# Performance work log

Hardware: AMD Instinct MI355X
Metric: run time of the kernel (lower is better)

Reference implementation:

```python
import jax, jax.numpy as jnp
import numpy as np

B, S, D, K, DF, H, DFF = 2, 512, 512, 8, 64, 8, 2048
DH = D // H  # d_head = 64
CS = D // K  # chunk_size = 64


def layer_norm(x, g, b, eps=1e-5):
    m = x.mean(-1, keepdims=True)
    v = ((x - m) ** 2).mean(-1, keepdims=True)
    return (x - m) / jnp.sqrt(v + eps) * g + b


def matexp_taylor(M, terms=6):
    # exp(M) ~= I + M + M^2/2! + ... (6 terms), batched over leading dims
    I = jnp.broadcast_to(jnp.eye(M.shape[-1], dtype=M.dtype), M.shape)
    res, P = I, I
    for n in range(1, terms + 1):
        P = jnp.matmul(P, M) / n
        res = res + P
    return res


def setup_inputs() -> dict:
    key = jax.random.key(0)
    ks = jax.random.split(key, 24)
    w = lambda k, shape, s=0.02: (jax.random.normal(k, shape, jnp.float32) * s)
    return {
        'x': jax.random.normal(ks[0], (B, S, D), jnp.float32),
        'u': jax.random.normal(ks[1], (B, S, DF), jnp.float32),
        'Wq': w(ks[2], (D, D)), 'bq': jnp.zeros((D,), jnp.float32),
        'Wk': w(ks[3], (D, D)), 'bk': jnp.zeros((D,), jnp.float32),
        'Wv': w(ks[4], (D, D)), 'bv': jnp.zeros((D,), jnp.float32),
        'Wo': w(ks[5], (D, D)), 'bo': jnp.zeros((D,), jnp.float32),
        'Wfp': w(ks[6], (DF, D)), 'bfp': jnp.zeros((D,), jnp.float32),
        'Wfo': w(ks[7], (D, DF)), 'bfo': jnp.zeros((DF,), jnp.float32),
        'Wc1': w(ks[8], (D, DFF)), 'bc1': jnp.zeros((DFF,), jnp.float32),
        'g_ln': jnp.ones((DFF,), jnp.float32), 'b_ln': jnp.zeros((DFF,), jnp.float32),
        # small scale keeps the Lie elements O(1) so the Taylor matexp is well-behaved
        'Wc2': w(ks[9], (DFF, D * K * K), 0.001), 'bc2': jnp.zeros((D * K * K,), jnp.float32),
    }


def reference(x, u, Wq, bq, Wk, bk, Wv, bv, Wo, bo, Wfp, bfp, Wfo, bfo,
              Wc1, bc1, g_ln, b_ln, Wc2, bc2):
    b, s, d = x.shape
    # --- ConnectionNetwork: A[b,s,d,k,k] ---
    h = jax.nn.gelu(x @ Wc1 + bc1, approximate=False)
    h = layer_norm(h, g_ln, b_ln)
    A = (h @ Wc2 + bc2).reshape(b, s, d, K, K)
    # --- ParallelTransport: lie[b,i,j] = sum_d (x_i - x_j)_d * A[j,d]  ---
    # (split into x_i.A_j and x_j.A_j terms to avoid [b,s,s,d,k,k] intermediate)
    lie = jnp.einsum('bid,bjdkl->bijkl', x, A) - jnp.einsum('bjd,bjdkl->bjkl', x, A)[:, None]
    Gamma = matexp_taylor(-lie)  # [b,s,s,k,k], Gamma[b,i,j] transports j->i
    # --- standard multi-head attention on x (eval mode, no dropout, no mask) ---
    q = (x @ Wq + bq).reshape(b, s, H, DH).transpose(0, 2, 1, 3)
    k_ = (x @ Wk + bk).reshape(b, s, H, DH).transpose(0, 2, 1, 3)
    v = (x @ Wv + bv).reshape(b, s, H, DH).transpose(0, 2, 1, 3)
    scores = jnp.einsum('bhid,bhjd->bhij', q, k_) / jnp.sqrt(jnp.float32(DH))
    attn = jax.nn.softmax(scores, axis=-1)
    ctx = jnp.einsum('bhij,bhjd->bhid', attn, v).transpose(0, 2, 1, 3).reshape(b, s, d)
    x_out = x + ctx @ Wo + bo
    # --- fiber transport: u_i += sum_j attn_avg[i,j] * Gamma[i,j] @ u_chunks[j] ---
    u_proj = u @ Wfp + bfp                      # [b,s,D]
    u_chunks = u_proj.reshape(b, s, K, CS)      # [b,s,k,cs]
    attn_avg = attn.mean(axis=1)                # [b,s,s]
    weighted = Gamma * attn_avg[..., None, None]
    u_t = jnp.einsum('bijkl,bjlc->bikc', weighted, u_chunks).reshape(b, s, d)
    u_out = u + u_t @ Wfo + bfo
    return (x_out, u_out)
```

## Files before the change

kernel.cpp:

```cpp
#include <hip/hip_runtime.h>
#include <math.h>

#define BB 2
#define SS 512
#define DD 512
#define HH 8
#define DFF 2048

typedef __attribute__((ext_vector_type(8))) short bf16x8;
typedef __attribute__((ext_vector_type(4))) float f32x4;

__device__ __forceinline__ float gelu_exact(float v) {
    return 0.5f * v * (1.0f + erff(v * 0.70710678118654752f));
}
__device__ __forceinline__ unsigned short f2bf(float f) {
    unsigned u = __float_as_uint(f);
    u += 0x7FFF + ((u >> 16) & 1);
    return (unsigned short)(u >> 16);
}
__device__ __forceinline__ float bf2f(unsigned short s) {
    return __uint_as_float(((unsigned)s) << 16);
}
__device__ __forceinline__ void gload16(const void* g, void* l) {
    __builtin_amdgcn_global_load_lds((const __attribute__((address_space(1))) void*)g,
                                     (__attribute__((address_space(3))) void*)l, 16, 0, 0);
}

template<int NT, int EPI, int SK = 1>
__global__ __launch_bounds__(256)
void mgemm_k(const unsigned short* __restrict__ A, const unsigned short* __restrict__ B,
             const float* __restrict__ bias, const float* __restrict__ resid,
             float* __restrict__ Cf, unsigned short* __restrict__ Cb,
             int K, int lda, int ldb, int ldc, int batchH,
             long aSB, long aSH, long bSB, long bSH, long cSB, long cSH,
             float scale)
{
    __shared__ unsigned short As[128][32];
    __shared__ unsigned short Bs[NT][32];
    const int tid = threadIdx.x;
    const int wave = tid >> 6, lane = tid & 63;
    const int z = blockIdx.z;
    const int zb = z / batchH, zh = z % batchH;
    const unsigned short* Ab = A + (long)zb * aSB + (long)zh * aSH;
    const unsigned short* Bb = B + (long)zb * bSB + (long)zh * bSH;
    const int chunk = (SK > 1) ? ((int)blockIdx.x % SK) : 0;
    const int colb  = (SK > 1) ? ((int)blockIdx.x / SK) : (int)blockIdx.x;
    const int row0 = blockIdx.y * 128, col0 = colb * NT;
    const int wm = wave >> 1, wn = wave & 1;
    const int lm = lane & 15, quad = lane >> 4;
    const int lrow = lane >> 2, lk = (lane & 3) * 8;
    constexpr int NTW = NT / 32;
    f32x4 acc[4][NTW];
    #pragma unroll
    for (int i = 0; i < 4; ++i)
        #pragma unroll
        for (int j = 0; j < NTW; ++j) acc[i][j] = (f32x4)0.f;

    const int kLo = chunk * (K / SK), kHi = kLo + K / SK;
    for (int k0 = kLo; k0 < kHi; k0 += 32) {
        #pragma unroll
        for (int t = 0; t < 2; ++t) {
            const int r = wave * 32 + t * 16;
            gload16(Ab + (long)(row0 + r + lrow) * lda + k0 + lk, &As[r][0]);
        }
        if (NT == 128) {
            #pragma unroll
            for (int t = 0; t < 2; ++t) {
                const int r = wave * 32 + t * 16;
                gload16(Bb + (long)(col0 + r + lrow) * ldb + k0 + lk, &Bs[r][0]);
            }
        } else {
            const int r = wave * 16;
            gload16(Bb + (long)(col0 + r + lrow) * ldb + k0 + lk, &Bs[r][0]);
        }
        __syncthreads();
        bf16x8 af[4], bfr[NTW];
        #pragma unroll
        for (int mt = 0; mt < 4; ++mt)
            af[mt] = *(const bf16x8*)&As[wm * 64 + mt * 16 + lm][quad * 8];
        #pragma unroll
        for (int nt = 0; nt < NTW; ++nt)
            bfr[nt] = *(const bf16x8*)&Bs[wn * (NT / 2) + nt * 16 + lm][quad * 8];
        #pragma unroll
        for (int mt = 0; mt < 4; ++mt)
            #pragma unroll
            for (int nt = 0; nt < NTW; ++nt)
                acc[mt][nt] = __builtin_amdgcn_mfma_f32_16x16x32_bf16(
                    af[mt], bfr[nt], acc[mt][nt], 0, 0, 0);
        __syncthreads();
    }
    float* Cfz = (Cf && EPI != 7) ? Cf + (long)zb * cSB + (long)zh * cSH : Cf;
    unsigned short* Cbz = Cb ? Cb + (long)zb * cSB + (long)zh * cSH : nullptr;
    #pragma unroll
    for (int mt = 0; mt < 4; ++mt) {
        #pragma unroll
        for (int nt = 0; nt < NTW; ++nt) {
            #pragma unroll
            for (int r = 0; r < 4; ++r) {
                const int row = row0 + wm * 64 + mt * 16 + quad * 4 + r;
                const int col = col0 + wn * (NT / 2) + nt * 16 + lm;
                float v = acc[mt][nt][r] * scale;
                if (EPI == 2)      v += bias[(col & 511) * 64 + (col >> 9)];
                else if (EPI == 1 || EPI == 4) v += bias[col];
                else if ((EPI == 3 || EPI == 5 || EPI == 6) && bias) v += bias[col];
                if (EPI == 1) v = gelu_exact(v);
                if (EPI == 4) v += resid[(long)row * ldc + col];
                if (EPI == 0 || EPI == 1 || EPI == 4)
                    Cfz[(long)row * ldc + col] = v;
                else if (EPI == 7)
                    Cf[(long)z * cSB + (long)chunk * cSH + (long)row * ldc + col] = v;
                else if (EPI == 2 || EPI == 3)
                    Cbz[(long)row * ldc + col] = f2bf(v);
                else if (EPI == 5)
                    Cb[(long)(row >> 9) * 262144 + (col >> 6) * 32768 +
                       (col & 63) * 512 + (row & 511)] = f2bf(v);
                else if (EPI == 6)
                    Cb[(long)(row >> 9) * 262144 + (col & 63) * 4096 +
                       (row & 511) * 8 + (col >> 6)] = f2bf(v);
            }
        }
    }
}

__global__ __launch_bounds__(256)
void redqkv_k(const float* __restrict__ p, const float* __restrict__ bq,
              const float* __restrict__ bk, const float* __restrict__ bv,
              unsigned short* __restrict__ q_bf, unsigned short* __restrict__ k_bf,
              unsigned short* __restrict__ vT)
{
    const int col = blockIdx.x * 256 + threadIdx.x;
    const int row = blockIdx.y;
    const long base = (long)row * 1536 + col;
    float s = p[base] + p[base + 1572864] + p[base + 3145728] + p[base + 4718592];
    const int which = col >> 9;
    const int scol = col & 511;
    if (which == 0) {
        q_bf[(long)row * 512 + scol] = f2bf(s + bq[scol]);
    } else if (which == 1) {
        k_bf[(long)row * 512 + scol] = f2bf(s + bk[scol]);
    } else {
        s += bv[scol];
        vT[(long)(row >> 9) * 262144 + (scol >> 6) * 32768 +
           (scol & 63) * 512 + (row & 511)] = f2bf(s);
    }
}
__global__ __launch_bounds__(256)
void redwo_k(const float* __restrict__ p, const float* __restrict__ bias,
             const float* __restrict__ resid, float* __restrict__ out)
{
    const long idx = (long)blockIdx.x * 256 + threadIdx.x;
    out[idx] = resid[idx] + bias[idx & 511]
             + p[idx] + p[idx + 524288] + p[idx + 1048576] + p[idx + 1572864];
}
template<int SK>
__global__ __launch_bounds__(256)
void redzc_k(const float* __restrict__ p, unsigned short* __restrict__ out)
{
    const long idx = (long)blockIdx.x * 256 + threadIdx.x;
    float s = 0.f;
    #pragma unroll
    for (int k = 0; k < SK; ++k) s += p[idx + (long)k * 524288];
    const int b = (int)(idx >> 18), zh = (int)((idx >> 15) & 7);
    const long rem = idx & 32767;
    const int i = (int)(rem >> 6), c = (int)(rem & 63);
    out[(long)b * 262144 + (long)i * 512 + zh * 64 + c] = f2bf(s);
}
__global__ __launch_bounds__(256)
void redu_k(const float* __restrict__ p, const float* __restrict__ bias,
            const float* __restrict__ resid, float* __restrict__ out)
{
    const long idx = (long)blockIdx.x * 256 + threadIdx.x;
    out[idx] = resid[idx] + bias[idx & 63]
             + p[idx] + p[idx + 65536] + p[idx + 131072] + p[idx + 196608];
}

__global__ __launch_bounds__(512, 2)
void fc2_k(const unsigned short* __restrict__ A, const unsigned short* __restrict__ Bm,
           const float* __restrict__ bias, unsigned short* __restrict__ C)
{
    extern __shared__ unsigned short smraw[];
#define SMA(ab, h) (smraw + (((ab) * 2 + (h)) * 8192))
#define SMB(bb, h) (smraw + (32768 + ((bb) * 2 + (h)) * 8192))
    const int tid = threadIdx.x;
    const int wave = tid >> 6, lane = tid & 63;
    const int bid = blockIdx.x;
    const int lin = (bid & 7) * 64 + (bid >> 3);
    const int by = lin & 3, bx = lin >> 2;
    const int row0 = by * 256, col0 = bx * 256;
    const int wm = wave >> 2, wn = wave & 3;
    const int lm = lane & 15, quad = lane >> 4;
    const int axor = lm & 7;
    const int arow = (wm * 64 + lm) * 64;
    const int brow = (wn * 32 + lm) * 64;
    const int ca0 = ((quad) ^ axor) * 8;
    const int ca1 = ((quad + 4) ^ axor) * 8;
    const int srow = wave * 8 + (lane >> 3);
    const int scx = ((lane & 7) ^ ((lane >> 3) & 7)) * 8;
    const int sbrow = ((srow >> 5) << 6) + (srow & 31);
    const unsigned short* AgB = A + (long)(row0 + srow) * 2048 + scx;
    const unsigned short* BgB = Bm + (long)(col0 + sbrow) * 2048 + scx;

    f32x4 acc[8][4];
    #pragma unroll
    for (int i = 0; i < 8; ++i)
        #pragma unroll
        for (int j = 0; j < 4; ++j) acc[i][j] = (f32x4)0.f;
    bf16x8 afr[4][2], b0f[2][2], b1f[2][2];

#define STGA(ab, h, toff) do { \
        const unsigned short* _g = AgB + (toff) * 64 + (h) * (64 * 2048); \
        unsigned short* _d = SMA(ab, h) + wave * 512; \
        gload16(_g, _d); \
        gload16(_g + 128 * 2048, _d + 4096); \
    } while (0)
#define STGB(bb, h, toff) do { \
        const unsigned short* _g = BgB + (toff) * 64 + (h) * (32 * 2048); \
        unsigned short* _d = SMB(bb, h) + wave * 512; \
        gload16(_g, _d); \
        gload16(_g + 128 * 2048, _d + 4096); \
    } while (0)
#define RDA(Hp) do { _Pragma("unroll") for (int _m = 0; _m < 4; ++_m) { \
        afr[_m][0] = *(const bf16x8*)((Hp) + arow + _m * 1024 + ca0); \
        afr[_m][1] = *(const bf16x8*)((Hp) + arow + _m * 1024 + ca1); } } while (0)
#define RDB(bf, Hp) do { _Pragma("unroll") for (int _n = 0; _n < 2; ++_n) { \
        bf[_n][0] = *(const bf16x8*)((Hp) + brow + _n * 1024 + ca0); \
        bf[_n][1] = *(const bf16x8*)((Hp) + brow + _n * 1024 + ca1); } } while (0)
#define MM(QM, QN, bf) do { _Pragma("unroll") for (int _m = 0; _m < 4; ++_m) \
        _Pragma("unroll") for (int _n = 0; _n < 2; ++_n) { \
        acc[(QM)*4+_m][(QN)*2+_n] = __builtin_amdgcn_mfma_f32_16x16x32_bf16( \
            afr[_m][0], bf[_n][0], acc[(QM)*4+_m][(QN)*2+_n], 0, 0, 0); \
        acc[(QM)*4+_m][(QN)*2+_n] = __builtin_amdgcn_mfma_f32_16x16x32_bf16( \
            afr[_m][1], bf[_n][1], acc[(QM)*4+_m][(QN)*2+_n], 0, 0, 0); } } while (0)
#define PH_MID() \
        __builtin_amdgcn_s_barrier(); \
        asm volatile("s_waitcnt lgkmcnt(0)" ::: "memory"); \
        __builtin_amdgcn_sched_barrier(0); \
        __builtin_amdgcn_s_setprio(1)
#define PH_END(VM) \
        __builtin_amdgcn_s_setprio(0); \
        __builtin_amdgcn_sched_barrier(0); \
        asm volatile("s_waitcnt vmcnt(" #VM ")" ::: "memory"); \
        __builtin_amdgcn_sched_barrier(0); \
        __builtin_amdgcn_s_barrier()
#define PH_END_NW() \
        __builtin_amdgcn_s_setprio(0); \
        __builtin_amdgcn_sched_barrier(0); \
        __builtin_amdgcn_s_barrier()

    STGB(0, 0, 0);
    STGB(0, 1, 0);
    STGA(0, 0, 0);
    STGA(0, 1, 0);
    STGB(1, 0, 1);
    STGB(1, 1, 1);
    asm volatile("s_waitcnt vmcnt(6)" ::: "memory");
    __builtin_amdgcn_s_barrier();

    int rA = 0;
    int rB = 0, mB = 1, wB = 2;
    #pragma unroll 1
    for (int t = 0; t < 32; ++t) {
        const int tA = (t + 1 < 32) ? (t + 1) : 31;
        const int tB = (t + 2 < 32) ? (t + 2) : 31;
        const unsigned short* A0p = SMA(rA, 0);
        const unsigned short* A1p = SMA(rA, 1);
        const unsigned short* B0p = SMB(rB, 0);
        const unsigned short* B1p = SMB(rB, 1);
        RDA(A0p); RDB(b0f, B0p);
        STGA(rA ^ 1, 0, tA);
        PH_MID(); MM(0, 0, b0f); PH_END_NW();
        RDB(b1f, B1p);
        STGA(rA ^ 1, 1, tA);
        PH_MID(); MM(0, 1, b1f); PH_END(8);
        RDA(A1p);
        STGB(wB, 0, tB);
        PH_MID(); MM(1, 1, b1f); PH_END_NW();
        STGB(wB, 1, tB);
        PH_MID(); MM(1, 0, b0f); PH_END(6);
        rA ^= 1;
        const int tmp = rB; rB = mB; mB = wB; wB = tmp;
    }
    asm volatile("s_waitcnt vmcnt(0)" ::: "memory");

    const int crow = row0 + wm * 128 + quad * 4;
    const int ccol0 = col0 + wn * 64 + lm;
    #pragma unroll
    for (int ms = 0; ms < 8; ++ms)
        #pragma unroll
        for (int ns = 0; ns < 4; ++ns) {
            const int col = ccol0 + ns * 16;
            const float bv = bias[(col & 511) * 64 + (col >> 9)];
            #pragma unroll
            for (int r = 0; r < 4; ++r) {
                const int row = crow + ms * 16 + r;
                C[(long)row * 32768 + col] = f2bf(acc[ms][ns][r] + bv);
            }
        }
#undef SMA
#undef SMB
#undef STGA
#undef STGB
#undef RDA
#undef RDB
#undef MM
#undef PH_MID
#undef PH_END
#undef PH_END_NW
}

__global__ __launch_bounds__(256)
void liegamma_k(const unsigned short* __restrict__ xb, const unsigned short* __restrict__ At,
                const float* __restrict__ xf, const float* __restrict__ aavg,
                unsigned short* __restrict__ Gw)
{
    __shared__ unsigned short Xs[128][32];
    __shared__ unsigned short Ts[64][32];
    __shared__ float Ml[128][68];
    __shared__ float xjs[512];
    __shared__ float xred[64][4];
    __shared__ float xafin[64];
    const int tid = threadIdx.x;
    const int wave = tid >> 6, lane = tid & 63;
    const int b = blockIdx.z, j = blockIdx.y;
    const int i0 = blockIdx.x * 128;
    const int lm = lane & 15, quad = lane >> 4;
    const int lrow = lane >> 2, lk = (lane & 3) * 8;
    const unsigned short* Xb = xb + ((long)b * 512 + i0) * 512;
    const unsigned short* Tb = At + ((long)(b * 512 + j)) * 32768;
    const float* xrow = xf + ((long)b * 512 + j) * 512;
    xjs[tid] = xrow[tid];
    xjs[tid + 256] = xrow[tid + 256];
    f32x4 acc[2][4];
    #pragma unroll
    for (int i = 0; i < 2; ++i)
        #pragma unroll
        for (int n = 0; n < 4; ++n) acc[i][n] = (f32x4)0.f;
    float xas = 0.f;
    const int kl2 = tid >> 2, q2 = tid & 3;

    for (int k0 = 0; k0 < 512; k0 += 32) {
        #pragma unroll
        for (int t = 0; t < 2; ++t) {
            const int r = wave * 32 + t * 16;
            gload16(Xb + (long)(r + lrow) * 512 + k0 + lk, &Xs[r][0]);
        }
        {
            const int r = wave * 16;
            gload16(Tb + (long)(r + lrow) * 512 + k0 + lk, &Ts[r][0]);
        }
        __syncthreads();
        bf16x8 af[2], bfr[4];
        #pragma unroll
        for (int mt = 0; mt < 2; ++mt)
            af[mt] = *(const bf16x8*)&Xs[wave * 32 + mt * 16 + lm][quad * 8];
        #pragma unroll
        for (int nt = 0; nt < 4; ++nt)
            bfr[nt] = *(const bf16x8*)&Ts[nt * 16 + lm][quad * 8];
        #pragma unroll
        for (int mt = 0; mt < 2; ++mt)
            #pragma unroll
            for (int nt = 0; nt < 4; ++nt)
                acc[mt][nt] = __builtin_amdgcn_mfma_f32_16x16x32_bf16(
                    af[mt], bfr[nt], acc[mt][nt], 0, 0, 0);
        {
            const bf16x8 tv = *(const bf16x8*)&Ts[kl2][q2 * 8];
            const float* xs = &xjs[k0 + q2 * 8];
            #pragma unroll
            for (int e = 0; e < 8; ++e)
                xas = fmaf(xs[e], bf2f((unsigned short)tv[e]), xas);
        }
        __syncthreads();
    }
    xred[kl2][q2] = xas;
    __syncthreads();
    if (tid < 64)
        xafin[tid] = xred[tid][0] + xred[tid][1] + xred[tid][2] + xred[tid][3];
    __syncthreads();
    #pragma unroll
    for (int mt = 0; mt < 2; ++mt)
        #pragma unroll
        for (int nt = 0; nt < 4; ++nt) {
            const float xv = xafin[nt * 16 + lm];
            #pragma unroll
            for (int r = 0; r < 4; ++r)
                Ml[wave * 32 + mt * 16 + quad * 4 + r][nt * 16 + lm] = xv - acc[mt][nt][r];
        }
    __syncthreads();
    const int r8 = tid & 7, mg = tid >> 3;
    #pragma unroll 1
    for (int pass = 0; pass < 4; ++pass) {
        const int mi = pass * 32 + mg;
        const f32x4* Mr = (const f32x4*)&Ml[mi][0];
        f32x4 Mreg[16];
        #pragma unroll
        for (int l = 0; l < 16; ++l) Mreg[l] = Mr[l];
        float P[8], res[8];
        #pragma unroll
        for (int c = 0; c < 8; ++c) { const float iv = (c == r8) ? 1.f : 0.f; P[c] = iv; res[c] = iv; }
        #pragma unroll
        for (int n = 1; n <= 6; ++n) {
            float tmp[8] = {0.f,0.f,0.f,0.f,0.f,0.f,0.f,0.f};
            const float invn = 1.f / (float)n;
            #pragma unroll
            for (int l = 0; l < 8; ++l) {
                const f32x4 m0 = Mreg[l * 2], m1 = Mreg[l * 2 + 1];
                const float pl = P[l];
                #pragma unroll
                for (int c = 0; c < 4; ++c) {
                    tmp[c]     = fmaf(pl, m0[c], tmp[c]);
                    tmp[4 + c] = fmaf(pl, m1[c], tmp[4 + c]);
                }
            }
            #pragma unroll
            for (int c = 0; c < 8; ++c) { P[c] = tmp[c] * invn; res[c] += P[c]; }
        }
        const float av = aavg[((long)b * 512 + i0 + mi) * 512 + j];
        bf16x8 o;
        #pragma unroll
        for (int c = 0; c < 8; ++c) o[c] = (short)f2bf(res[c] * av);
        *(bf16x8*)(Gw + ((long)(b * 8 + r8) * 512 + (i0 + mi)) * 4096 + (long)j * 8) = o;
    }
}

__global__ __launch_bounds__(256)
void lnbf_k(const float* __restrict__ h, const float* __restrict__ g,
            const float* __restrict__ b, unsigned short* __restrict__ out)
{
    const long row = blockIdx.x;
    const float* r = h + row * (long)DFF;
    const int tid = threadIdx.x;
    float vals[8];
    float s = 0.f, sq = 0.f;
    #pragma unroll
    for (int e = 0; e < 8; ++e) {
        const float v = r[tid + e * 256];
        vals[e] = v; s += v; sq += v * v;
    }
    __shared__ float rs[256], rq[256];
    rs[tid] = s; rq[tid] = sq; __syncthreads();
    for (int st = 128; st > 0; st >>= 1) {
        if (tid < st) { rs[tid] += rs[tid + st]; rq[tid] += rq[tid + st]; }
        __syncthreads();
    }
    const float mean = rs[0] * (1.f / DFF);
    const float var  = rq[0] * (1.f / DFF) - mean * mean;
    const float inv  = rsqrtf(var + 1e-5f);
    unsigned short* o = out + row * (long)DFF;
    #pragma unroll
    for (int e = 0; e < 8; ++e) {
        const int c = tid + e * 256;
        o[c] = f2bf((vals[e] - mean) * inv * g[c] + b[c]);
    }
}

__global__ __launch_bounds__(256)
void softmax_k(float* __restrict__ p, unsigned short* __restrict__ pb)
{
    const long row = blockIdx.x;
    float* r = p + row * 512;
    const int tid = threadIdx.x;
    float v0 = r[tid], v1 = r[tid + 256];
    __shared__ float red[256];
    red[tid] = fmaxf(v0, v1); __syncthreads();
    for (int s = 128; s > 0; s >>= 1) {
        if (tid < s) red[tid] = fmaxf(red[tid], red[tid + s]);
        __syncthreads();
    }
    const float m = red[0]; __syncthreads();
    v0 = expf(v0 - m); v1 = expf(v1 - m);
    red[tid] = v0 + v1; __syncthreads();
    for (int s = 128; s > 0; s >>= 1) {
        if (tid < s) red[tid] += red[tid + s];
        __syncthreads();
    }
    const float inv = 1.f / red[0];
    const float a0 = v0 * inv, a1 = v1 * inv;
    r[tid] = a0; r[tid + 256] = a1;
    unsigned short* rb = pb + row * 512;
    rb[tid] = f2bf(a0); rb[tid + 256] = f2bf(a1);
}

__global__ __launch_bounds__(256)
void aavg_k(const float* __restrict__ attn, float* __restrict__ aavg)
{
    const long idx = (long)blockIdx.x * 256 + threadIdx.x;
    const int b = (int)(idx >> 18);
    const long rem = idx & 262143;
    float s = 0.f;
    #pragma unroll
    for (int h = 0; h < HH; ++h)
        s += attn[(long)b * 2097152 + (long)h * 262144 + rem];
    aavg[idx] = s * 0.125f;
}

__global__ __launch_bounds__(256)
void tconv_k(const float* __restrict__ in, unsigned short* __restrict__ out,
             int R, int C)
{
    __shared__ float Ls[64][65];
    const int c0 = blockIdx.x * 64, r0 = blockIdx.y * 64;
    const int tid = threadIdx.x;
    const int tc = tid & 63, tr = tid >> 6;
    #pragma unroll
    for (int p = 0; p < 16; ++p)
        Ls[tr + p * 4][tc] = in[(long)(r0 + tr + p * 4) * C + c0 + tc];
    __syncthreads();
    #pragma unroll
    for (int p = 0; p < 16; ++p)
        out[(long)(c0 + tr + p * 4) * R + r0 + tc] = f2bf(Ls[tc][tr + p * 4]);
}

__global__ __launch_bounds__(256)
void tconv4_k(const float* __restrict__ W0, const float* __restrict__ W1,
              const float* __restrict__ W2, const float* __restrict__ W3,
              unsigned short* __restrict__ outbase)
{
    __shared__ float Ls[64][65];
    const int z = blockIdx.z;
    const float* in = (z == 0) ? W0 : (z == 1) ? W1 : (z == 2) ? W2 : W3;
    unsigned short* out = outbase + (long)z * 262144;
    const int c0 = blockIdx.x * 64, r0 = blockIdx.y * 64;
    const int tid = threadIdx.x;
    const int tc = tid & 63, tr = tid >> 6;
    #pragma unroll
    for (int p = 0; p < 16; ++p)
        Ls[tr + p * 4][tc] = in[(long)(r0 + tr + p * 4) * 512 + c0 + tc];
    __syncthreads();
    #pragma unroll
    for (int p = 0; p < 16; ++p)
        out[(long)(c0 + tr + p * 4) * 512 + r0 + tc] = f2bf(Ls[tc][tr + p * 4]);
}

__global__ __launch_bounds__(256)
void wc2p_k(const float* __restrict__ in, unsigned short* __restrict__ out)
{
    __shared__ float Ls[64][65];
    const int d0 = blockIdx.x;
    const long f0 = blockIdx.y * 64;
    const int tid = threadIdx.x;
    const int tc = tid & 63, tr = tid >> 6;
    #pragma unroll
    for (int p = 0; p < 16; ++p)
        Ls[tr + p * 4][tc] = in[(f0 + tr + p * 4) * 32768 + (long)d0 * 64 + tc];
    __syncthreads();
    #pragma unroll
    for (int p = 0; p < 16; ++p) {
        const int kl = tr + p * 4;
        out[((long)kl * 512 + d0) * 2048 + f0 + tc] = f2bf(Ls[tc][kl]);
    }
}

__global__ __launch_bounds__(256)
void f2bf_k(const float* __restrict__ in, unsigned short* __restrict__ out, int n)
{
    const int i = blockIdx.x * 256 + threadIdx.x;
    if (i < n) out[i] = f2bf(in[i]);
}

extern "C" void kernel_launch(void* const* d_in, const int* in_sizes, int n_in,
                              void* d_out, int out_size, void* d_ws, size_t ws_size,
                              hipStream_t stream) {
    const float* x   = (const float*)d_in[0];
    const float* u   = (const float*)d_in[1];
    const float* Wq  = (const float*)d_in[2];  const float* bq  = (const float*)d_in[3];
    const float* Wk  = (const float*)d_in[4];  const float* bk  = (const float*)d_in[5];
    const float* Wv  = (const float*)d_in[6];  const float* bv  = (const float*)d_in[7];
    const float* Wo  = (const float*)d_in[8];  const float* bo  = (const float*)d_in[9];
    const float* Wfp = (const float*)d_in[10]; const float* bfp = (const float*)d_in[11];
    const float* Wfo = (const float*)d_in[12]; const float* bfo = (const float*)d_in[13];
    const float* Wc1 = (const float*)d_in[14]; const float* bc1 = (const float*)d_in[15];
    const float* gln = (const float*)d_in[16]; const float* bln = (const float*)d_in[17];
    const float* Wc2 = (const float*)d_in[18]; const float* bc2 = (const float*)d_in[19];

    float* ws = (float*)d_ws;
    unsigned short* Wc2p = (unsigned short*)(ws);
    unsigned short* Gw   = (unsigned short*)(ws);
    unsigned short* At   = (unsigned short*)(ws + 33554432);
    float*          h    = ws + 50331648;
    unsigned short* h_bf = (unsigned short*)(ws + 52428800);
    unsigned short* x_bf = (unsigned short*)(ws + 53477376);
    unsigned short* u_bf = (unsigned short*)(ws + 53739520);
    unsigned short* Wc1t = (unsigned short*)(ws + 53772288);
    unsigned short* Wqt  = (unsigned short*)(ws + 54296576);
    unsigned short* Wkt  = (unsigned short*)(ws + 54427648);
    unsigned short* Wvt  = (unsigned short*)(ws + 54558720);
    unsigned short* Wot  = (unsigned short*)(ws + 54689792);
    unsigned short* Wfpt = (unsigned short*)(ws + 54820864);
    unsigned short* Wfot = (unsigned short*)(ws + 54837248);
    float*          xa   = ws + 54853632;
    unsigned short* q_bf = (unsigned short*)(ws + 54919168);
    unsigned short* k_bf = (unsigned short*)(ws + 55181312);
    unsigned short* vT   = (unsigned short*)(ws + 55443456);
    float*          sc   = ws + 55705600;
    unsigned short* at_bf= (unsigned short*)(ws + 59899904);
    float*          av   = ws + 61997056;
    unsigned short* ctx  = (unsigned short*)(ws + 62521344);
    unsigned short* upT2 = (unsigned short*)(ws + 62783488);
    unsigned short* ut_bf= (unsigned short*)(ws + 63045632);
    float*          qkvp = ws + 63307776;
    float*          wop  = ws + 69599232;
    float*          ctxp = ws + 71696384;
    float*          utp  = ws + 73793536;
    float*          up   = ws + 77987840;
    float* xout = (float*)d_out;
    float* uout = xout + 524288;
    (void)xa;

    const dim3 blk(256);

    hipFuncSetAttribute(reinterpret_cast<const void*>(fc2_k),
                        hipFuncAttributeMaxDynamicSharedMemorySize, 163840);

    tconv_k<<<dim3(32, 8), blk, 0, stream>>>(Wc1, Wc1t, 512, 2048);
    tconv4_k<<<dim3(8, 8, 4), blk, 0, stream>>>(Wq, Wk, Wv, Wo, Wqt);
    tconv_k<<<dim3(8, 1), blk, 0, stream>>>(Wfp, Wfpt, 64, 512);
    tconv_k<<<dim3(1, 8), blk, 0, stream>>>(Wfo, Wfot, 512, 64);
    wc2p_k<<<dim3(512, 32), blk, 0, stream>>>(Wc2, Wc2p);
    f2bf_k<<<dim3(2048), blk, 0, stream>>>(x, x_bf, 524288);
    f2bf_k<<<dim3(256), blk, 0, stream>>>(u, u_bf, 65536);

    mgemm_k<128,7,4><<<dim3(48, 8, 1), blk, 0, stream>>>(
        x_bf, Wqt, nullptr, nullptr, qkvp, nullptr, 512, 512, 512, 1536,
        1, 0,0,0,0, 0,1572864, 1.0f);
    redqkv_k<<<dim3(6, 1024), blk, 0, stream>>>(qkvp, bq, bk, bv, q_bf, k_bf, vT);
    mgemm_k<128,0><<<dim3(4, 4, 16), blk, 0, stream>>>(
        q_bf, k_bf, nullptr, nullptr, sc, nullptr, 64, 512, 512, 512,
        8, 262144,64, 262144,64, 2097152,262144, 0.125f);
    softmax_k<<<dim3(BB * HH * SS), blk, 0, stream>>>(sc, at_bf);
    aavg_k<<<dim3(2048), blk, 0, stream>>>(sc, av);
    mgemm_k<64,7,4><<<dim3(4, 4, 16), blk, 0, stream>>>(
        at_bf, vT, nullptr, nullptr, ctxp, nullptr, 512, 512, 512, 64,
        8, 2097152,262144, 262144,32768, 32768,524288, 1.0f);
    redzc_k<4><<<dim3(2048), blk, 0, stream>>>(ctxp, ctx);
    mgemm_k<128,7,4><<<dim3(16, 8, 1), blk, 0, stream>>>(
        ctx, Wot, nullptr, nullptr, wop, nullptr, 512, 512, 512, 512,
        1, 0,0,0,0, 0,524288, 1.0f);
    redwo_k<<<dim3(2048), blk, 0, stream>>>(wop, bo, x, xout);

    mgemm_k<128,1><<<dim3(16, 8, 1), blk, 0, stream>>>(
        x_bf, Wc1t, bc1, nullptr, h, nullptr, 512, 512, 512, 2048,
        1, 0,0,0,0,0,0, 1.0f);
    lnbf_k<<<dim3(1024), blk, 0, stream>>>(h, gln, bln, h_bf);
    fc2_k<<<dim3(512), dim3(512), 163840, stream>>>(h_bf, Wc2p, bc2, At);
    liegamma_k<<<dim3(4, 512, 2), blk, 0, stream>>>(x_bf, At, x, av, Gw);

    mgemm_k<128,6><<<dim3(4, 8, 1), blk, 0, stream>>>(
        u_bf, Wfpt, bfp, nullptr, nullptr, upT2, 64, 64, 64, 512,
        1, 0,0,0,0,0,0, 1.0f);
    mgemm_k<64,7,8><<<dim3(8, 4, 16), blk, 0, stream>>>(
        Gw, upT2, nullptr, nullptr, utp, nullptr, 4096, 4096, 4096, 64,
        8, 16777216,2097152, 262144,0, 32768,524288, 1.0f);
    redzc_k<8><<<dim3(2048), blk, 0, stream>>>(utp, ut_bf);
    mgemm_k<64,7,4><<<dim3(4, 8, 1), blk, 0, stream>>>(
        ut_bf, Wfot, nullptr, nullptr, up, nullptr, 512, 512, 512, 64,
        1, 0,0,0,0, 0,65536, 1.0f);
    redu_k<<<dim3(256), blk, 0, stream>>>(up, bfo, u, uout);
}
```

Baseline: 822.9 us.

## Fuse QK^T scores and softmax into one attention kernel writing bf16 probabilities

```diff
diff --git a/kernel.cpp b/kernel.cpp
--- a/kernel.cpp
+++ b/kernel.cpp
@@ -172,6 +172,145 @@
     const long idx = (long)blockIdx.x * 256 + threadIdx.x;
     out[idx] = resid[idx] + bias[idx & 63]
              + p[idx] + p[idx + 65536] + p[idx + 131072] + p[idx + 196608];
+}
+
+__global__ __launch_bounds__(512)
+void attn_k(const unsigned short* __restrict__ q_bf, const unsigned short* __restrict__ k_bf,
+            unsigned short* __restrict__ at)
+{
+    extern __shared__ unsigned short sm[];
+    unsigned short* Qs = sm;
+    unsigned short* Ks = sm + 4096;
+    float* redm = (float*)(sm + 36864);
+    float* rowv = redm + 512;
+    const int tid = threadIdx.x;
+    const int wave = tid >> 6, lane = tid & 63;
+    const int lm = lane & 15, quad = lane >> 4;
+    const int z = blockIdx.y, h = z & 7, b = z >> 3;
+    const int i0 = blockIdx.x * 64;
+    const unsigned short* Qg = q_bf + (long)b * 262144;
+    const unsigned short* Kg = k_bf + (long)b * 262144;
+    const int srow = wave * 8 + (lane >> 3);
+    const int scx = ((lane & 7) ^ ((lane >> 3) & 7)) * 8;
+    gload16(Qg + (long)(i0 + srow) * 512 + h * 64 + scx, Qs + wave * 512);
+    #pragma unroll
+    for (int p = 0; p < 8; ++p)
+        gload16(Kg + (long)(p * 64 + srow) * 512 + h * 64 + scx,
+                Ks + p * 4096 + wave * 512);
+    asm volatile("s_waitcnt vmcnt(0)" ::: "memory");
+    __syncthreads();
+
+    const int axor = lm & 7;
+    const int ca0 = ((quad) ^ axor) * 8;
+    const int ca1 = ((quad + 4) ^ axor) * 8;
+    bf16x8 af[4][2], bfk[4][2];
+    #pragma unroll
+    for (int mt = 0; mt < 4; ++mt) {
+        af[mt][0] = *(const bf16x8*)&Qs[(mt * 16 + lm) * 64 + ca0];
+        af[mt][1] = *(const bf16x8*)&Qs[(mt * 16 + lm) * 64 + ca1];
+    }
+    #pragma unroll
+    for (int nt = 0; nt < 4; ++nt) {
+        bfk[nt][0] = *(const bf16x8*)&Ks[(wave * 64 + nt * 16 + lm) * 64 + ca0];
+        bfk[nt][1] = *(const bf16x8*)&Ks[(wave * 64 + nt * 16 + lm) * 64 + ca1];
+    }
+    f32x4 acc[4][4];
+    #pragma unroll
+    for (int i = 0; i < 4; ++i)
+        #pragma unroll
+        for (int j = 0; j < 4; ++j) acc[i][j] = (f32x4)0.f;
+    #pragma unroll
+    for (int mt = 0; mt < 4; ++mt)
+        #pragma unroll
+        for (int nt = 0; nt < 4; ++nt) {
+            acc[mt][nt] = __builtin_amdgcn_mfma_f32_16x16x32_bf16(
+                af[mt][0], bfk[nt][0], acc[mt][nt], 0, 0, 0);
+            acc[mt][nt] = __builtin_amdgcn_mfma_f32_16x16x32_bf16(
+                af[mt][1], bfk[nt][1], acc[mt][nt], 0, 0, 0);
+        }
+    #pragma unroll
+    for (int mt = 0; mt < 4; ++mt)
+        #pragma unroll
+        for (int nt = 0; nt < 4; ++nt)
+            #pragma unroll
+            for (int r = 0; r < 4; ++r) acc[mt][nt][r] *= 0.125f;
+    #pragma unroll
+    for (int mt = 0; mt < 4; ++mt)
+        #pragma unroll
+        for (int r = 0; r < 4; ++r) {
+            float m = fmaxf(fmaxf(acc[mt][0][r], acc[mt][1][r]),
+                            fmaxf(acc[mt][2][r], acc[mt][3][r]));
+            m = fmaxf(m, __shfl_xor(m, 1));
+            m = fmaxf(m, __shfl_xor(m, 2));
+            m = fmaxf(m, __shfl_xor(m, 4));
+            m = fmaxf(m, __shfl_xor(m, 8));
+            if (lm == 0) redm[(mt * 16 + quad * 4 + r) * 8 + wave] = m;
+        }
+    __syncthreads();
+    if (tid < 64) {
+        float m = redm[tid * 8];
+        #pragma unroll
+        for (int w = 1; w < 8; ++w) m = fmaxf(m, redm[tid * 8 + w]);
+        rowv[tid] = m;
+    }
+    __syncthreads();
+    #pragma unroll
+    for (int mt = 0; mt < 4; ++mt)
+        #pragma unroll
+        for (int r = 0; r < 4; ++r) {
+            const float rm = rowv[mt * 16 + quad * 4 + r];
+            float s = 0.f;
+            #pragma unroll
+            for (int nt = 0; nt < 4; ++nt) {
+                const float e = expf(acc[mt][nt][r] - rm);
+                acc[mt][nt][r] = e; s += e;
+            }
+            s += __shfl_xor(s, 1);
+            s += __shfl_xor(s, 2);
+            s += __shfl_xor(s, 4);
+            s += __shfl_xor(s, 8);
+            if (lm == 0) redm[(mt * 16 + quad * 4 + r) * 8 + wave] = s;
+        }
+    __syncthreads();
+    if (tid < 64) {
+        float s = redm[tid * 8];
+        #pragma unroll
+        for (int w = 1; w < 8; ++w) s += redm[tid * 8 + w];
+        rowv[tid] = 1.f / s;
+    }
+    __syncthreads();
+    unsigned short* ao = at + (long)z * 262144;
+    #pragma unroll
+    for (int mt = 0; mt < 4; ++mt)
+        #pragma unroll
+        for (int r = 0; r < 4; ++r) {
+            const int row = mt * 16 + quad * 4 + r;
+            const float inv = rowv[row];
+            #pragma unroll
+            for (int nt = 0; nt < 4; ++nt)
+                ao[(long)(i0 + row) * 512 + wave * 64 + nt * 16 + lm] =
+                    f2bf(acc[mt][nt][r] * inv);
+        }
+}
+
+__global__ __launch_bounds__(256)
+void aavg_k(const unsigned short* __restrict__ at, float* __restrict__ av)
+{
+    const long idx4 = ((long)blockIdx.x * 256 + threadIdx.x) * 4;
+    const int b = (int)(idx4 >> 18);
+    const long rem = idx4 & 262143;
+    float s0 = 0.f, s1 = 0.f, s2 = 0.f, s3 = 0.f;
+    #pragma unroll
+    for (int h = 0; h < HH; ++h) {
+        const unsigned long long w = *(const unsigned long long*)
+            &at[(long)b * 2097152 + (long)h * 262144 + rem];
+        s0 += bf2f((unsigned short)(w));
+        s1 += bf2f((unsigned short)(w >> 16));
+        s2 += bf2f((unsigned short)(w >> 32));
+        s3 += bf2f((unsigned short)(w >> 48));
+    }
+    f32x4 o; o[0] = s0 * 0.125f; o[1] = s1 * 0.125f; o[2] = s2 * 0.125f; o[3] = s3 * 0.125f;
+    *(f32x4*)&av[idx4] = o;
 }
 
 __global__ __launch_bounds__(512, 2)
@@ -454,46 +593,6 @@
 }
 
 __global__ __launch_bounds__(256)
-void softmax_k(float* __restrict__ p, unsigned short* __restrict__ pb)
-{
-    const long row = blockIdx.x;
-    float* r = p + row * 512;
-    const int tid = threadIdx.x;
-    float v0 = r[tid], v1 = r[tid + 256];
-    __shared__ float red[256];
-    red[tid] = fmaxf(v0, v1); __syncthreads();
-    for (int s = 128; s > 0; s >>= 1) {
-        if (tid < s) red[tid] = fmaxf(red[tid], red[tid + s]);
-        __syncthreads();
-    }
-    const float m = red[0]; __syncthreads();
-    v0 = expf(v0 - m); v1 = expf(v1 - m);
-    red[tid] = v0 + v1; __syncthreads();
-    for (int s = 128; s > 0; s >>= 1) {
-        if (tid < s) red[tid] += red[tid + s];
-        __syncthreads();
-    }
-    const float inv = 1.f / red[0];
-    const float a0 = v0 * inv, a1 = v1 * inv;
-    r[tid] = a0; r[tid + 256] = a1;
-    unsigned short* rb = pb + row * 512;
-    rb[tid] = f2bf(a0); rb[tid + 256] = f2bf(a1);
-}
-
-__global__ __launch_bounds__(256)
-void aavg_k(const float* __restrict__ attn, float* __restrict__ aavg)
-{
-    const long idx = (long)blockIdx.x * 256 + threadIdx.x;
-    const int b = (int)(idx >> 18);
-    const long rem = idx & 262143;
-    float s = 0.f;
-    #pragma unroll
-    for (int h = 0; h < HH; ++h)
-        s += attn[(long)b * 2097152 + (long)h * 262144 + rem];
-    aavg[idx] = s * 0.125f;
-}
-
-__global__ __launch_bounds__(256)
 void tconv_k(const float* __restrict__ in, unsigned short* __restrict__ out,
              int R, int C)
 {
@@ -532,6 +631,28 @@
 }
 
 __global__ __launch_bounds__(256)
+void tconvfp_k(const float* __restrict__ Wfp, const float* __restrict__ Wfo,
+               unsigned short* __restrict__ ofp, unsigned short* __restrict__ ofo)
+{
+    __shared__ float Ls[64][65];
+    const int z = blockIdx.z;
+    const float* in = z ? Wfo : Wfp;
+    unsigned short* out = z ? ofo : ofp;
+    const int R = z ? 512 : 64, C = z ? 64 : 512;
+    const int c0 = z ? 0 : blockIdx.x * 64;
+    const int r0 = z ? blockIdx.x * 64 : 0;
+    const int tid = threadIdx.x;
+    const int tc = tid & 63, tr = tid >> 6;
+    #pragma unroll
+    for (int p = 0; p < 16; ++p)
+        Ls[tr + p * 4][tc] = in[(long)(r0 + tr + p * 4) * C + c0 + tc];
+    __syncthreads();
+    #pragma unroll
+    for (int p = 0; p < 16; ++p)
+        out[(long)(c0 + tr + p * 4) * R + r0 + tc] = f2bf(Ls[tc][tr + p * 4]);
+}
+
+__global__ __launch_bounds__(256)
 void wc2p_k(const float* __restrict__ in, unsigned short* __restrict__ out)
 {
     __shared__ float Ls[64][65];
@@ -551,10 +672,17 @@
 }
 
 __global__ __launch_bounds__(256)
-void f2bf_k(const float* __restrict__ in, unsigned short* __restrict__ out, int n)
-{
-    const int i = blockIdx.x * 256 + threadIdx.x;
-    if (i < n) out[i] = f2bf(in[i]);
+void f2bfxu_k(const float* __restrict__ x, const float* __restrict__ u,
+              unsigned short* __restrict__ xo, unsigned short* __restrict__ uo)
+{
+    const int bid = blockIdx.x;
+    if (bid < 2048) {
+        const int i = bid * 256 + threadIdx.x;
+        xo[i] = f2bf(x[i]);
+    } else {
+        const int i = (bid - 2048) * 256 + threadIdx.x;
+        uo[i] = f2bf(u[i]);
+    }
 }
 
 extern "C" void kernel_launch(void* const* d_in, const int* in_sizes, int n_in,
@@ -587,11 +715,9 @@
     unsigned short* Wot  = (unsigned short*)(ws + 54689792);
     unsigned short* Wfpt = (unsigned short*)(ws + 54820864);
     unsigned short* Wfot = (unsigned short*)(ws + 54837248);
-    float*          xa   = ws + 54853632;
     unsigned short* q_bf = (unsigned short*)(ws + 54919168);
     unsigned short* k_bf = (unsigned short*)(ws + 55181312);
     unsigned short* vT   = (unsigned short*)(ws + 55443456);
-    float*          sc   = ws + 55705600;
     unsigned short* at_bf= (unsigned short*)(ws + 59899904);
     float*          av   = ws + 61997056;
     unsigned short* ctx  = (unsigned short*)(ws + 62521344);
@@ -604,30 +730,26 @@
     float*          up   = ws + 77987840;
     float* xout = (float*)d_out;
     float* uout = xout + 524288;
-    (void)xa;
 
     const dim3 blk(256);
 
     hipFuncSetAttribute(reinterpret_cast<const void*>(fc2_k),
                         hipFuncAttributeMaxDynamicSharedMemorySize, 163840);
+    hipFuncSetAttribute(reinterpret_cast<const void*>(attn_k),
+                        hipFuncAttributeMaxDynamicSharedMemorySize, 76800);
 
     tconv_k<<<dim3(32, 8), blk, 0, stream>>>(Wc1, Wc1t, 512, 2048);
     tconv4_k<<<dim3(8, 8, 4), blk, 0, stream>>>(Wq, Wk, Wv, Wo, Wqt);
-    tconv_k<<<dim3(8, 1), blk, 0, stream>>>(Wfp, Wfpt, 64, 512);
-    tconv_k<<<dim3(1, 8), blk, 0, stream>>>(Wfo, Wfot, 512, 64);
+    tconvfp_k<<<dim3(8, 1, 2), blk, 0, stream>>>(Wfp, Wfo, Wfpt, Wfot);
     wc2p_k<<<dim3(512, 32), blk, 0, stream>>>(Wc2, Wc2p);
-    f2bf_k<<<dim3(2048), blk, 0, stream>>>(x, x_bf, 524288);
-    f2bf_k<<<dim3(256), blk, 0, stream>>>(u, u_bf, 65536);
+    f2bfxu_k<<<dim3(2304), blk, 0, stream>>>(x, u, x_bf, u_bf);
 
     mgemm_k<128,7,4><<<dim3(48, 8, 1), blk, 0, stream>>>(
         x_bf, Wqt, nullptr, nullptr, qkvp, nullptr, 512, 512, 512, 1536,
         1, 0,0,0,0, 0,1572864, 1.0f);
     redqkv_k<<<dim3(6, 1024), blk, 0, stream>>>(qkvp, bq, bk, bv, q_bf, k_bf, vT);
-    mgemm_k<128,0><<<dim3(4, 4, 16), blk, 0, stream>>>(
-        q_bf, k_bf, nullptr, nullptr, sc, nullptr, 64, 512, 512, 512,
-        8, 262144,64, 262144,64, 2097152,262144, 0.125f);
-    softmax_k<<<dim3(BB * HH * SS), blk, 0, stream>>>(sc, at_bf);
-    aavg_k<<<dim3(2048), blk, 0, stream>>>(sc, av);
+    attn_k<<<dim3(8, 16), dim3(512), 76800, stream>>>(q_bf, k_bf, at_bf);
+    aavg_k<<<dim3(512), blk, 0, stream>>>(at_bf, av);
     mgemm_k<64,7,4><<<dim3(4, 4, 16), blk, 0, stream>>>(
         at_bf, vT, nullptr, nullptr, ctxp, nullptr, 512, 512, 512, 64,
         8, 2097152,262144, 262144,32768, 32768,524288, 1.0f);
```

Result: no change. 814.1 us (-1.1%).
